# Performance work log

Hardware: AMD Instinct MI355X
Metric: run time of the kernel (lower is better)

Reference implementation:

```python
import jax, jax.numpy as jnp
import numpy as np
from functools import partial

B, L = 8, 2500          # batch, note length
V = 50002               # vocab + 2
E = 100                 # embed_size
F = 50                  # num_filter_maps
K = 9                   # kernel_size (padding = 4)
Y = 8922                # number of ICD codes (Y4)


def setup_inputs() -> dict:
    key = jax.random.key(0)
    ks = jax.random.split(key, 12)
    x = jax.random.randint(ks[0], (B, L), 0, 50000, dtype=jnp.int64)
    target = jnp.zeros((B, Y), dtype=jnp.float32)
    embed_w = jax.random.normal(ks[1], (V, E), dtype=jnp.float32) * 0.1
    embed_w = embed_w.at[0].set(0.0)  # padding_idx=0
    conv_w = jax.random.normal(ks[2], (F, E, K), dtype=jnp.float32) * (1.0 / np.sqrt(E * K))
    conv_b = jnp.zeros((F,), dtype=jnp.float32)
    U4_w = jax.random.normal(ks[3], (Y, F), dtype=jnp.float32) * (1.0 / np.sqrt(F))
    gcn_w = jax.random.normal(ks[4], (F, F), dtype=jnp.float32) * (1.0 / np.sqrt(F))
    gcn_b = jax.random.uniform(ks[5], (F,), dtype=jnp.float32, minval=-1/np.sqrt(F), maxval=1/np.sqrt(F))
    # normalized co-occurrence adjacency (row-stochastic-ish, fixed buffer)
    adj = jax.random.uniform(ks[6], (Y, Y), dtype=jnp.float32)
    adj = adj / jnp.sum(adj, axis=1, keepdims=True)
    final4t_w = jax.random.normal(ks[7], (Y, F), dtype=jnp.float32) * (1.0 / np.sqrt(F))
    final4t_b = jnp.zeros((Y,), dtype=jnp.float32)
    final4_w = jax.random.normal(ks[8], (Y, 2 * F), dtype=jnp.float32) * (1.0 / np.sqrt(2 * F))
    final4_b = jnp.zeros((Y,), dtype=jnp.float32)
    return {
        "x": x, "target": target,
        "embed_w": embed_w, "conv_w": conv_w, "conv_b": conv_b,
        "U4_w": U4_w, "gcn_w": gcn_w, "gcn_b": gcn_b, "adj": adj,
        "final4t_w": final4t_w, "final4t_b": final4t_b,
        "final4_w": final4_w, "final4_b": final4_b,
    }


def reference(x, target, embed_w, conv_w, conv_b, U4_w, gcn_w, gcn_b, adj,
              final4t_w, final4t_b, final4_w, final4_b):
    # embedding (dropout is identity at inference)
    emb = embed_w[x]                              # [B, L, E]
    # conv1d over sequence: NCH layout, same padding
    h = jax.lax.conv_general_dilated(
        emb.transpose(0, 2, 1), conv_w,
        window_strides=(1,), padding=[(K // 2, K // 2)],
        dimension_numbers=("NCH", "OIH", "NCH"))
    hp = jnp.tanh(h.transpose(0, 2, 1) + conv_b)  # [B, L, F]
    # per-label attention over sequence
    scores = jnp.einsum("yf,blf->byl", U4_w, hp)  # [B, Y, L]
    alpha4 = jax.nn.softmax(scores, axis=-1)
    m4t = jnp.einsum("byl,blf->byf", alpha4, hp)  # [B, Y, F]
    # graph conv over label co-occurrence graph
    support = jnp.einsum("byf,fg->byg", m4t, gcn_w)
    out1 = jnp.einsum("yz,bzg->byg", adj, support) + gcn_b
    out1 = jax.nn.leaky_relu(out1, negative_slope=0.2)
    m4 = jnp.concatenate([m4t, out1], axis=2)     # [B, Y, 2F]
    # label-wise linear scoring
    y4t = jnp.einsum("byf,yf->by", m4t, final4t_w) + final4t_b
    y4 = jnp.einsum("byf,yf->by", m4, final4_w) + final4_b
    return y4t, y4
```

## Files before the change

kernel.cpp:

```cpp
#include <hip/hip_runtime.h>

typedef unsigned short u16;
typedef short bf16x8 __attribute__((ext_vector_type(8)));
typedef float f32x4  __attribute__((ext_vector_type(4)));
typedef u16   u16x8  __attribute__((ext_vector_type(8)));

#define MFMA_BF16(a, b, c) __builtin_amdgcn_mfma_f32_16x16x32_bf16((a), (b), (c), 0, 0, 0)

#define B_  8
#define L_  2500
#define LP  2528
#define E_  100
#define F_  50
#define Y_  8922
#define YP  8960
#define KT_ 280
#define NT_ 416
#define KP_ 4
#define AMAX_ (Y_ * Y_ - 1)

__device__ __forceinline__ u16 f2bf(float f) {
    unsigned int x = __float_as_uint(f);
    unsigned int r = x + 0x7fffu + ((x >> 16) & 1u);
    return (u16)(r >> 16);
}

__device__ __forceinline__ void glds16(const void* g, const void* l) {
    __builtin_amdgcn_global_load_lds(
        (const __attribute__((address_space(1))) unsigned int*)(unsigned long long)g,
        (__attribute__((address_space(3))) unsigned int*)(unsigned int)(unsigned long long)l,
        16, 0, 0);
}
__device__ __forceinline__ void glds4(const void* g, const void* l) {
    __builtin_amdgcn_global_load_lds(
        (const __attribute__((address_space(1))) unsigned int*)(unsigned long long)g,
        (__attribute__((address_space(3))) unsigned int*)(unsigned int)(unsigned long long)l,
        4, 0, 0);
}

__global__ __launch_bounds__(256) void k0_prep(
    const int* __restrict__ x, const float* __restrict__ conv_w,
    int* __restrict__ flag, float* __restrict__ wT)
{
    const int k = blockIdx.x;
    const int tid = threadIdx.x;
    if (k == 0 && tid == 0) {
        int nz = 0;
        #pragma unroll
        for (int i = 0; i < 32; i++) nz |= x[2 * i + 1];
        *flag = (nz == 0) ? 1 : 0;
    }
    for (int j = tid; j < 5000; j += 256)
        wT[k * 5000 + j] = conv_w[j * 9 + k];
}

__global__ __launch_bounds__(256) void k1_conv(
    const int* __restrict__ x, const int* __restrict__ flag,
    const float* __restrict__ embed_w, const float* __restrict__ wT,
    const float* __restrict__ conv_b,
    u16* __restrict__ hp, u16* __restrict__ hpT)
{
    __shared__ float sEmb[72 * 104];
    __shared__ float sW[50 * 104];
    __shared__ int   sId[72];
    const int tid = threadIdx.x;
    const int b  = blockIdx.y;
    const int l0 = blockIdx.x * 64;
    const int is64 = *flag;

    if (tid < 72) {
        int l = l0 - 4 + tid;
        int id = -1;
        if (l >= 0 && l < L_) id = is64 ? x[(b * L_ + l) * 2] : x[b * L_ + l];
        sId[tid] = id;
    }
    __syncthreads();
    for (int i = tid; i < 72 * 25; i += 256) {
        int r = i / 25, e4 = i - r * 25;
        int id = sId[r];
        float4 v = make_float4(0.f, 0.f, 0.f, 0.f);
        if (id >= 0) v = *(const float4*)&embed_w[(size_t)id * 100 + e4 * 4];
        *(float4*)&sEmb[r * 104 + e4 * 4] = v;
    }

    const int li = tid & 63;
    const int fg = __builtin_amdgcn_readfirstlane(tid >> 6);

    float acc[13];
    #pragma unroll
    for (int i = 0; i < 13; i++) { int f = fg + 4 * i; acc[i] = (f < F_) ? conv_b[f] : 0.f; }

    for (int k = 0; k < 9; k++) {
        __syncthreads();
        for (int i = tid; i < 1250; i += 256) {
            int f = i / 25, e4 = i - f * 25;
            *(float4*)&sW[f * 104 + e4 * 4] = *(const float4*)&wT[k * 5000 + f * 100 + e4 * 4];
        }
        __syncthreads();
        for (int e4 = 0; e4 < 25; e4++) {
            float4 h = *(const float4*)&sEmb[(li + k) * 104 + e4 * 4];
            #pragma unroll
            for (int i = 0; i < 13; i++) {
                int f = fg + 4 * i;
                if (f < F_) {
                    float4 w = *(const float4*)&sW[f * 104 + e4 * 4];
                    acc[i] += h.x * w.x + h.y * w.y + h.z * w.z + h.w * w.w;
                }
            }
        }
    }

    int l = l0 + li;
    if (l < LP) {
        bool valid = (l < L_);
        #pragma unroll
        for (int i = 0; i < 13; i++) {
            int f = fg + 4 * i;
            if (f < F_) {
                u16 hv = 0;
                if (valid) {
                    float e2 = __expf(2.f * acc[i]);
                    hv = f2bf((e2 - 1.f) / (e2 + 1.f));
                }
                hp [((size_t)b * LP + l) * 64 + f] = hv;
                hpT[((size_t)b * 64 + f) * LP + l] = hv;
            }
        }
        #pragma unroll
        for (int j = 0; j < 4; j++) {
            int f = 50 + fg + 4 * j;
            if (f < 64) {
                hp [((size_t)b * LP + l) * 64 + f] = 0;
                hpT[((size_t)b * 64 + f) * LP + l] = (f == 50 && valid) ? f2bf(1.f) : (u16)0;
            }
        }
    }
}

__global__ __launch_bounds__(256) void k2_attn(
    const float* __restrict__ U4_w,
    const u16* __restrict__ hp, const u16* __restrict__ hpT,
    float* __restrict__ m4t)
{
    __shared__ u16  sU4[128 * 72];
    __shared__ u16  sHp[32 * 72];
    __shared__ u16  sHt[64 * 40];
    __shared__ u16  sP [128 * 40];
    __shared__ float sDen[128];

    const int tid  = threadIdx.x;
    const int b    = blockIdx.y;
    const int y0   = blockIdx.x * 128;
    const int w    = tid >> 6;
    const int lane = tid & 63;
    const int l15  = lane & 15;
    const int quad = lane >> 4;

    for (int i = tid; i < 128 * 72; i += 256) {
        int r = i / 72, c = i - r * 72;
        float v = 0.f;
        int y = y0 + r;
        if (c < F_ && y < Y_) v = U4_w[y * F_ + c];
        sU4[i] = f2bf(v);
    }
    __syncthreads();

    bf16x8 fa[2][2];
    #pragma unroll
    for (int mi = 0; mi < 2; mi++)
        #pragma unroll
        for (int ks = 0; ks < 2; ks++)
            fa[mi][ks] = *(const bf16x8*)&sU4[(w * 32 + mi * 16 + l15) * 72 + ks * 32 + quad * 8];

    const f32x4 fz = {0.f, 0.f, 0.f, 0.f};
    f32x4 pacc[2][4];
    #pragma unroll
    for (int mi = 0; mi < 2; mi++)
        #pragma unroll
        for (int ni = 0; ni < 4; ni++) pacc[mi][ni] = fz;

    const int rr = tid >> 3, seg = tid & 7;
    const int fr = tid >> 2, s2 = tid & 3;
    u16x8 pv, pv2;
    {
        pv  = *(const u16x8*)&hp [((size_t)b * LP + rr) * 64 + seg * 8];
        pv2 = *(const u16x8*)&hpT[((size_t)b * 64 + fr) * LP + s2 * 8];
    }

    for (int lt = 0; lt < 79; lt++) {
        const int l0 = lt * 32;
        __syncthreads();
        *(u16x8*)&sHp[rr * 72 + seg * 8] = pv;
        *(u16x8*)&sHt[fr * 40 + s2 * 8] = pv2;
        if (lt + 1 < 79) {
            const int ln = l0 + 32;
            pv  = *(const u16x8*)&hp [((size_t)b * LP + ln + rr) * 64 + seg * 8];
            pv2 = *(const u16x8*)&hpT[((size_t)b * 64 + fr) * LP + ln + s2 * 8];
        }
        __syncthreads();

        f32x4 sacc[2][2];
        #pragma unroll
        for (int mi = 0; mi < 2; mi++)
            #pragma unroll
            for (int ni = 0; ni < 2; ni++) sacc[mi][ni] = fz;
        #pragma unroll
        for (int ks = 0; ks < 2; ks++) {
            #pragma unroll
            for (int ni = 0; ni < 2; ni++) {
                bf16x8 fb = *(const bf16x8*)&sHp[(ni * 16 + l15) * 72 + ks * 32 + quad * 8];
                #pragma unroll
                for (int mi = 0; mi < 2; mi++)
                    sacc[mi][ni] = MFMA_BF16(fa[mi][ks], fb, sacc[mi][ni]);
            }
        }
        #pragma unroll
        for (int mi = 0; mi < 2; mi++)
            #pragma unroll
            for (int ni = 0; ni < 2; ni++) {
                int lcol = ni * 16 + l15;
                bool lv = (l0 + lcol) < L_;
                #pragma unroll
                for (int r = 0; r < 4; r++) {
                    float p = lv ? __expf(sacc[mi][ni][r]) : 0.f;
                    sP[(w * 32 + mi * 16 + quad * 4 + r) * 40 + lcol] = f2bf(p);
                }
            }
        __syncthreads();

        bf16x8 fv[4];
        #pragma unroll
        for (int ni = 0; ni < 4; ni++)
            fv[ni] = *(const bf16x8*)&sHt[(ni * 16 + l15) * 40 + quad * 8];
        #pragma unroll
        for (int mi = 0; mi < 2; mi++) {
            bf16x8 fp_ = *(const bf16x8*)&sP[(w * 32 + mi * 16 + l15) * 40 + quad * 8];
            #pragma unroll
            for (int ni = 0; ni < 4; ni++)
                pacc[mi][ni] = MFMA_BF16(fp_, fv[ni], pacc[mi][ni]);
        }
    }

    if (l15 == 2) {
        #pragma unroll
        for (int mi = 0; mi < 2; mi++)
            #pragma unroll
            for (int r = 0; r < 4; r++)
                sDen[w * 32 + mi * 16 + quad * 4 + r] = pacc[mi][3][r];
    }
    __syncthreads();

    #pragma unroll
    for (int mi = 0; mi < 2; mi++)
        #pragma unroll
        for (int ni = 0; ni < 4; ni++) {
            int f = ni * 16 + l15;
            if (f < F_) {
                #pragma unroll
                for (int r = 0; r < 4; r++) {
                    int yl = w * 32 + mi * 16 + quad * 4 + r;
                    int y = y0 + yl;
                    if (y < Y_)
                        m4t[((size_t)b * Y_ + y) * F_ + f] = pacc[mi][ni][r] / sDen[yl];
                }
            }
        }
}

__global__ __launch_bounds__(256) void k3_support(
    const float* __restrict__ m4t, const float* __restrict__ gcn_w,
    const float* __restrict__ f4t_w, const float* __restrict__ f4t_b,
    u16* __restrict__ Bt, float* __restrict__ y4t_out)
{
    __shared__ float sW[50 * 52];
    const int tid = threadIdx.x;
    for (int i = tid; i < 50 * 52; i += 256) {
        int g = i / 52, f = i - g * 52;
        sW[i] = (f < F_) ? gcn_w[f * F_ + g] : 0.f;
    }
    __syncthreads();

    const int b = blockIdx.y;
    const int y = blockIdx.x * 256 + tid;
    if (y >= Y_) return;

    float2 m[25];
    const float* mrow = m4t + ((size_t)b * Y_ + y) * F_;
    #pragma unroll
    for (int i = 0; i < 25; i++) m[i] = *(const float2*)(mrow + 2 * i);

    const int kt = y >> 5, zo = y & 31;
    const int zhi = zo >> 3, zlo = zo & 7;
    u16* btile = Bt + (size_t)kt * (NT_ * 32);
    for (int g = 0; g < F_; g++) {
        float s = 0.f;
        const float* wr = sW + g * 52;
        #pragma unroll
        for (int i = 0; i < 25; i++) {
            float2 wv = *(const float2*)(wr + 2 * i);
            s += m[i].x * wv.x + m[i].y * wv.y;
        }
        int n = b * F_ + g;
        btile[n * 32 + ((zhi ^ ((n >> 1) & 3)) << 3) + zlo] = f2bf(s);
    }

    const float* tw = f4t_w + (size_t)y * F_;
    float acc = f4t_b[y];
    #pragma unroll
    for (int i = 0; i < 25; i++) {
        float2 wv = *(const float2*)(tw + 2 * i);
        acc += m[i].x * wv.x + m[i].y * wv.y;
    }
    y4t_out[(size_t)b * Y_ + y] = acc;
}

__global__ __launch_bounds__(256, 3) void k4_gemm(
    const float* __restrict__ adj, const u16* __restrict__ Bt,
    float* __restrict__ outp)
{
    __shared__ float sA[64 * 32];
    __shared__ u16   sB[NT_ * 32];

    const int tid  = threadIdx.x;
    const int bid  = blockIdx.x;
    const int xcd  = bid & 7;
    const int kp   = xcd >> 1;
    const int mIdx = (bid >> 3) * 2 + (xcd & 1);
    const int m0   = mIdx * 64;
    const int w    = tid >> 6;
    const int wq   = __builtin_amdgcn_readfirstlane(w);
    const int lane = tid & 63;
    const int l15  = lane & 15;
    const int quad = lane >> 4;
    const int wm   = w & 1;
    const int wn   = w >> 1;

    const int rA   = tid >> 5;
    const int colA = ((((tid & 31) >> 2) ^ rA) << 2) | (tid & 3);
    const unsigned rbaseA = (unsigned)(m0 + rA) * (unsigned)Y_ + (unsigned)colA;

    const int r7    = l15 & 7;
    const int offA0 = (((2 * quad)     ^ r7) << 2);
    const int offA1 = (((2 * quad + 1) ^ r7) << 2);
    const int offB  = ((quad ^ ((l15 >> 1) & 3)) << 3);

    char* sAb = (char*)sA;
    char* sBb = (char*)sB;

    const f32x4 fz = {0.f, 0.f, 0.f, 0.f};
    f32x4 acc[2][13];
    #pragma unroll
    for (int mi = 0; mi < 2; mi++)
        #pragma unroll
        for (int ni = 0; ni < 13; ni++) acc[mi][ni] = fz;

    for (int it = 0; it < 70; it++) {
        const int kt = kp * 70 + it;
        __syncthreads();
        {
            const char* bt = (const char*)Bt + (size_t)kt * (NT_ * 32 * 2) + tid * 16;
            #pragma unroll
            for (int j = 0; j < 6; j++)
                glds16(bt + j * 4096, sBb + j * 4096 + wq * 1024);
            if (wq < 2)
                glds16(bt + 24576, sBb + 24576 + wq * 1024);
        }
        {
            const unsigned idx0 = rbaseA + (unsigned)kt * 32u;
            #pragma unroll
            for (int j = 0; j < 8; j++) {
                unsigned idx = idx0 + (unsigned)(j * 8 * Y_);
                idx = (idx > (unsigned)AMAX_) ? (unsigned)AMAX_ : idx;
                glds4(adj + idx, sAb + j * 1024 + wq * 256);
            }
        }
        __syncthreads();

        bf16x8 fa[2];
        #pragma unroll
        for (int mi = 0; mi < 2; mi++) {
            const int rb = (wm * 32 + mi * 16 + l15) * 32;
            f32x4 a0 = *(const f32x4*)&sA[rb + offA0];
            f32x4 a1 = *(const f32x4*)&sA[rb + offA1];
            bf16x8 v;
            v[0] = (short)f2bf(a0[0]); v[1] = (short)f2bf(a0[1]);
            v[2] = (short)f2bf(a0[2]); v[3] = (short)f2bf(a0[3]);
            v[4] = (short)f2bf(a1[0]); v[5] = (short)f2bf(a1[1]);
            v[6] = (short)f2bf(a1[2]); v[7] = (short)f2bf(a1[3]);
            fa[mi] = v;
        }
        #pragma unroll
        for (int ni = 0; ni < 13; ni++) {
            bf16x8 fb = *(const bf16x8*)&sB[(wn * 208 + ni * 16 + l15) * 32 + offB];
            acc[0][ni] = MFMA_BF16(fa[0], fb, acc[0][ni]);
            acc[1][ni] = MFMA_BF16(fa[1], fb, acc[1][ni]);
        }
    }

    float* dst = outp + (size_t)kp * Y_ * 400;
    #pragma unroll
    for (int mi = 0; mi < 2; mi++)
        #pragma unroll
        for (int ni = 0; ni < 13; ni++) {
            int n = wn * 208 + ni * 16 + l15;
            if (n < 400) {
                #pragma unroll
                for (int r4 = 0; r4 < 4; r4++) {
                    int y = m0 + wm * 32 + mi * 16 + quad * 4 + r4;
                    if (y < Y_) dst[(size_t)y * 400 + n] = acc[mi][ni][r4];
                }
            }
        }
}

__global__ __launch_bounds__(256) void k5_final(
    const float* __restrict__ outp, const float* __restrict__ m4t,
    const float* __restrict__ gcn_b, const float* __restrict__ f4_w,
    const float* __restrict__ f4_b, float* __restrict__ y4_out)
{
    const int b = blockIdx.y;
    const int y = blockIdx.x * 256 + threadIdx.x;
    if (y >= Y_) return;

    const size_t PS = (size_t)Y_ * 400;
    const float* p0 = outp + (size_t)y * 400 + b * F_;
    const float* fw = f4_w + (size_t)y * 100;
    const float* mrow = m4t + ((size_t)b * Y_ + y) * F_;

    float acc = f4_b[y];
    #pragma unroll
    for (int i = 0; i < 25; i++) {
        float2 mv = *(const float2*)(mrow + 2 * i);
        float2 wv = *(const float2*)(fw + 2 * i);
        acc += mv.x * wv.x + mv.y * wv.y;
    }
    #pragma unroll
    for (int i = 0; i < 25; i++) {
        float sx = 0.f, sy = 0.f;
        #pragma unroll
        for (int kp = 0; kp < KP_; kp++) {
            float2 v = *(const float2*)(p0 + kp * PS + 2 * i);
            sx += v.x; sy += v.y;
        }
        float2 gb = *(const float2*)(gcn_b + 2 * i);
        sx += gb.x; sy += gb.y;
        sx = sx > 0.f ? sx : 0.2f * sx;
        sy = sy > 0.f ? sy : 0.2f * sy;
        float2 wv = *(const float2*)(fw + 50 + 2 * i);
        acc += sx * wv.x + sy * wv.y;
    }
    y4_out[(size_t)b * Y_ + y] = acc;
}

extern "C" void kernel_launch(void* const* d_in, const int* in_sizes, int n_in,
                              void* d_out, int out_size, void* d_ws, size_t ws_size,
                              hipStream_t stream) {
    const int*   x       = (const int*)d_in[0];
    const float* embed_w = (const float*)d_in[2];
    const float* conv_w  = (const float*)d_in[3];
    const float* conv_b  = (const float*)d_in[4];
    const float* U4_w    = (const float*)d_in[5];
    const float* gcn_w   = (const float*)d_in[6];
    const float* gcn_b   = (const float*)d_in[7];
    const float* adj     = (const float*)d_in[8];
    const float* f4t_w   = (const float*)d_in[9];
    const float* f4t_b   = (const float*)d_in[10];
    const float* f4_w    = (const float*)d_in[11];
    const float* f4_b    = (const float*)d_in[12];
    float* out = (float*)d_out;

    char* ws = (char*)d_ws;
    const size_t SZ_WT  = 180224;
    const size_t SZ_HP  = (size_t)B_ * LP * 64 * 2;
    const size_t SZ_BT  = (size_t)KT_ * NT_ * 32 * 2;
    const size_t SZ_M4T = (size_t)B_ * Y_ * F_ * 4;
    int*   flag = (int*)ws;
    float* wT   = (float*)(ws + 16);
    u16*   hp   = (u16*)(ws + 16 + SZ_WT);
    u16*   hpT  = (u16*)(ws + 16 + SZ_WT + SZ_HP);
    u16*   Bt   = (u16*)(ws + 16 + SZ_WT + 2 * SZ_HP);
    float* m4t  = (float*)(ws + 16 + SZ_WT + 2 * SZ_HP + SZ_BT);
    float* outp = (float*)(ws + 16 + SZ_WT + 2 * SZ_HP + SZ_BT + SZ_M4T);

    k0_prep<<<9, 256, 0, stream>>>(x, conv_w, flag, wT);
    k1_conv<<<dim3(40, 8), 256, 0, stream>>>(x, flag, embed_w, wT, conv_b, hp, hpT);
    hipMemsetAsync(Bt, 0, SZ_BT, stream);
    k2_attn<<<dim3(70, 8), 256, 0, stream>>>(U4_w, hp, hpT, m4t);
    k3_support<<<dim3(35, 8), 256, 0, stream>>>(m4t, gcn_w, f4t_w, f4t_b, Bt, out);
    k4_gemm<<<dim3(140 * KP_), 256, 0, stream>>>(adj, Bt, outp);
    k5_final<<<dim3(35, 8), 256, 0, stream>>>(outp, m4t, gcn_b, f4_w, f4_b,
                                              out + (size_t)B_ * Y_);
}
```

Baseline: 975.4 us.

## Double-buffer LDS tiles in adjacency GEMM to overlap loads with MFMA

Splits the shared-memory A and B tiles of the adj x support GEMM into two buffers and prefetches the next K-tile with direct global-to-LDS loads while MFMAs run on the current one. Manual vmcnt waits and raw s_barriers replace the two __syncthreads per iteration. The aim is to hide global load latency behind compute. The cost is doubled LDS use, so launch bounds drop from 3 to 2 blocks per CU and occupancy falls. The partial B tile is also reloaded with 4-byte loads instead of 16-byte ones.

```diff
diff --git a/kernel.cpp b/kernel.cpp
--- a/kernel.cpp
+++ b/kernel.cpp
@@ -314,12 +314,12 @@
     y4t_out[(size_t)b * Y_ + y] = acc;
 }
 
-__global__ __launch_bounds__(256, 3) void k4_gemm(
+__global__ __launch_bounds__(256, 2) void k4_gemm(
     const float* __restrict__ adj, const u16* __restrict__ Bt,
     float* __restrict__ outp)
 {
-    __shared__ float sA[64 * 32];
-    __shared__ u16   sB[NT_ * 32];
+    __shared__ float sA[2][64 * 32];
+    __shared__ u16   sB[2][NT_ * 32];
 
     const int tid  = threadIdx.x;
     const int bid  = blockIdx.x;
@@ -344,9 +344,6 @@
     const int offA1 = (((2 * quad + 1) ^ r7) << 2);
     const int offB  = ((quad ^ ((l15 >> 1) & 3)) << 3);
 
-    char* sAb = (char*)sA;
-    char* sBb = (char*)sB;
-
     const f32x4 fz = {0.f, 0.f, 0.f, 0.f};
     f32x4 acc[2][13];
     #pragma unroll
@@ -354,34 +351,47 @@
         #pragma unroll
         for (int ni = 0; ni < 13; ni++) acc[mi][ni] = fz;
 
+    auto stage = [&](int buf, int kt) {
+        const char* bt = (const char*)Bt + (size_t)kt * (NT_ * 32 * 2);
+        char* sb = (char*)sB[buf];
+        #pragma unroll
+        for (int j = 0; j < 6; j++)
+            glds16(bt + j * 4096 + tid * 16, sb + j * 4096 + wq * 1024);
+        #pragma unroll
+        for (int j = 0; j < 2; j++)
+            glds4(bt + 24576 + j * 1024 + tid * 4, sb + 24576 + j * 1024 + wq * 256);
+        char* sa = (char*)sA[buf];
+        const unsigned idx0 = rbaseA + (unsigned)kt * 32u;
+        #pragma unroll
+        for (int j = 0; j < 8; j++) {
+            unsigned idx = idx0 + (unsigned)(j * 8 * Y_);
+            idx = (idx > (unsigned)AMAX_) ? (unsigned)AMAX_ : idx;
+            glds4(adj + idx, sa + j * 1024 + wq * 256);
+        }
+    };
+
+    const int kt0 = kp * 70;
+    stage(0, kt0);
+
     for (int it = 0; it < 70; it++) {
-        const int kt = kp * 70 + it;
-        __syncthreads();
-        {
-            const char* bt = (const char*)Bt + (size_t)kt * (NT_ * 32 * 2) + tid * 16;
-            #pragma unroll
-            for (int j = 0; j < 6; j++)
-                glds16(bt + j * 4096, sBb + j * 4096 + wq * 1024);
-            if (wq < 2)
-                glds16(bt + 24576, sBb + 24576 + wq * 1024);
-        }
-        {
-            const unsigned idx0 = rbaseA + (unsigned)kt * 32u;
-            #pragma unroll
-            for (int j = 0; j < 8; j++) {
-                unsigned idx = idx0 + (unsigned)(j * 8 * Y_);
-                idx = (idx > (unsigned)AMAX_) ? (unsigned)AMAX_ : idx;
-                glds4(adj + idx, sAb + j * 1024 + wq * 256);
-            }
-        }
-        __syncthreads();
-
+        const int cur = it & 1;
+        if (it + 1 < 70) {
+            stage(cur ^ 1, kt0 + it + 1);
+            asm volatile("s_waitcnt vmcnt(16)" ::: "memory");
+        } else {
+            asm volatile("s_waitcnt vmcnt(0)" ::: "memory");
+        }
+        __builtin_amdgcn_s_barrier();
+        __builtin_amdgcn_sched_barrier(0);
+
+        const float* sAc = sA[cur];
+        const u16*   sBc = sB[cur];
         bf16x8 fa[2];
         #pragma unroll
         for (int mi = 0; mi < 2; mi++) {
             const int rb = (wm * 32 + mi * 16 + l15) * 32;
-            f32x4 a0 = *(const f32x4*)&sA[rb + offA0];
-            f32x4 a1 = *(const f32x4*)&sA[rb + offA1];
+            f32x4 a0 = *(const f32x4*)&sAc[rb + offA0];
+            f32x4 a1 = *(const f32x4*)&sAc[rb + offA1];
             bf16x8 v;
             v[0] = (short)f2bf(a0[0]); v[1] = (short)f2bf(a0[1]);
             v[2] = (short)f2bf(a0[2]); v[3] = (short)f2bf(a0[3]);
@@ -391,10 +401,14 @@
         }
         #pragma unroll
         for (int ni = 0; ni < 13; ni++) {
-            bf16x8 fb = *(const bf16x8*)&sB[(wn * 208 + ni * 16 + l15) * 32 + offB];
+            bf16x8 fb = *(const bf16x8*)&sBc[(wn * 208 + ni * 16 + l15) * 32 + offB];
             acc[0][ni] = MFMA_BF16(fa[0], fb, acc[0][ni]);
             acc[1][ni] = MFMA_BF16(fa[1], fb, acc[1][ni]);
         }
+
+        __builtin_amdgcn_sched_barrier(0);
+        asm volatile("s_waitcnt lgkmcnt(0)" ::: "memory");
+        __builtin_amdgcn_s_barrier();
     }
 
     float* dst = outp + (size_t)kp * Y_ * 400;
```

Result: no change. 967.1 us (-0.9%).
